# Performance work log

Hardware: AMD Instinct MI355X
Metric: run time of the kernel (lower is better)

## Reference

```python
import jax, jax.numpy as jnp
import numpy as np

B, L, D, H = 8, 2048, 1024, 1024
BASE_LR, BASE_WD = 0.01, 0.9


def setup_inputs() -> dict:
    key = jax.random.key(0)
    ks = jax.random.split(key, 8)
    s = 1.0 / np.sqrt(D)
    return {
        "x": jax.random.normal(ks[0], (B, L, D), jnp.float32),
        "hidden": jax.random.normal(ks[1], (B, D, H), jnp.float32),
        "log_base_lr": jnp.array([np.log(BASE_LR)], jnp.float32),
        "w_lr": jax.random.normal(ks[2], (D, 1), jnp.float32) * s,
        "b_lr": jnp.zeros((1,), jnp.float32),
        "log_base_wd": jnp.array([np.log(BASE_WD)], jnp.float32),
        "w_wd": jax.random.normal(ks[3], (D, 1), jnp.float32) * s,
        "b_wd": jnp.zeros((1,), jnp.float32),
        "w_q": jax.random.normal(ks[4], (D, H), jnp.float32) * s,
        "b_q": jnp.zeros((H,), jnp.float32),
        "w_k": jax.random.normal(ks[5], (D, H), jnp.float32) * s,
        "b_k": jnp.zeros((H,), jnp.float32),
        "w_v": jax.random.normal(ks[6], (D, D), jnp.float32) * s,
        "b_v": jnp.zeros((D,), jnp.float32),
    }


def reference(x, hidden, log_base_lr, w_lr, b_lr, log_base_wd, w_wd, b_wd,
              w_q, b_q, w_k, b_k, w_v, b_v):
    batch, length, dim = x.shape
    W_prev = hidden  # [b, d, h]
    query = x @ w_q + b_q                     # [b, l, h]
    key = x @ w_k + b_k                       # [b, l, h]
    value = x @ w_v + b_v                     # [b, l, d]
    lr = jnp.exp(log_base_lr) * jax.nn.sigmoid((x @ w_lr + b_lr)[..., 0])  # [b, l]
    # log(1 - base_wd * sigmoid(.)) via log1p for stability; same math.
    log_wd = jnp.log1p(-jnp.exp(log_base_wd) * jax.nn.sigmoid((x @ w_wd + b_wd)[..., 0]))  # [b, l]
    wd_cross = jnp.exp(jnp.cumsum(log_wd, axis=1))  # [b, l]
    # inner-chunk decay: entry [b, m, l] = exp(sum_{j=m+1..l} log_wd[b, j]) for l >= m
    tri = jnp.triu(jnp.broadcast_to(log_wd[:, None, :], (batch, length, length)), k=1)
    wd_inner = jnp.triu(jnp.exp(jnp.cumsum(tri, axis=2)))  # [b, l, l]
    kq = jnp.einsum('bld,bmd->blm', key, query)            # [b, l, m]
    mask_kq = kq * wd_inner
    WpK_V = jnp.einsum('bdh,blh->bld', W_prev, key) - value  # [b, l, d]
    y_inner = -jnp.einsum('bld,bl,blm->bmd', WpK_V, lr, mask_kq)
    y_cross = jnp.einsum('bdh,blh,bl->bld', W_prev, query, wd_cross)
    y = y_inner + y_cross
    W_next_inner = -jnp.einsum('bld,bl,blh->bdh', WpK_V, lr * wd_inner[:, :, -1], key)
    W_next_cross = W_prev * wd_cross[:, -1][:, None, None]
    W_next = W_next_inner + W_next_cross
    return y, W_next
```

## Files before the change

kernel.cpp:

```cpp
#include <hip/hip_runtime.h>
#include <stdint.h>

#define BB 8
#define LL 2048
#define DD 1024
#define HH 1024
#define BL (BB*LL)

typedef __attribute__((ext_vector_type(8))) short short8;
typedef __attribute__((ext_vector_type(4))) float f32x4;

__device__ __forceinline__ unsigned short f2bf(float f) {
  unsigned int x = __float_as_uint(f);
  unsigned int r = (x + 0x7fffu + ((x >> 16) & 1u)) >> 16;
  return (unsigned short)r;
}
__device__ __forceinline__ float bf2f(unsigned short u) {
  return __uint_as_float(((unsigned int)u) << 16);
}

__device__ __forceinline__ void stage16(const unsigned short* g, unsigned short* l) {
  __builtin_amdgcn_global_load_lds((const __attribute__((address_space(1))) void*)g,
                                   (__attribute__((address_space(3))) void*)l,
                                   16, 0, 0);
}

template<int N> struct WaitVm;
#define WVM(N) template<> struct WaitVm<N> { \
  static __device__ __forceinline__ void w() { \
    asm volatile("s_waitcnt vmcnt(" #N ")" ::: "memory"); } };
WVM(0) WVM(6) WVM(8) WVM(12)
#undef WVM

template<int MI, int PD>
struct __align__(16) Smem3 {
  unsigned short a[PD+1][MI*2048];
  unsigned short b[PD+1][16384];
};

template<int MI>
__device__ __forceinline__ void acc_init2(f32x4 (&acc)[MI][4]) {
#pragma unroll
  for (int i = 0; i < MI; ++i)
#pragma unroll
    for (int j = 0; j < 4; ++j)
      acc[i][j] = (f32x4){0.f, 0.f, 0.f, 0.f};
}

template<int MI, int PD, class FA, class FB>
__device__ __forceinline__ void gemm3_core(FA srcA, FB srcB, int NK,
                                           Smem3<MI,PD>* sm, f32x4 (&acc)[MI][4]) {
  constexpr int NB  = PD + 1;
  constexpr int APW = MI / 2;
  constexpr int LPW = APW + 4;
  const int lane = threadIdx.x & 63;
  const int wave = threadIdx.x >> 6;
  const int srow = lane >> 3;
  const int scol = ((lane & 7) ^ srow) * 8;
  const int fk = (lane >> 4) * 8;
  const int fr = lane & 15;
  const int fx = fr & 7;
  const int mwr = (wave >> 2) * (MI * 16);
  const int nwr = (wave & 3) * 64;

  auto STAGE = [&](int p, int kt) {
#pragma unroll
    for (int r = 0; r < APW; ++r) {
      const int chunk = wave * APW + r;
      stage16(srcA(chunk * 8 + srow, kt) + scol, &sm->a[p][chunk * 512]);
    }
#pragma unroll
    for (int r = 0; r < 4; ++r) {
      const int chunk = wave * 4 + r;
      stage16(srcB(chunk * 8 + srow, kt) + scol, &sm->b[p][chunk * 512]);
    }
  };
  auto COMPUTE = [&](int p) {
    const unsigned short* pa  = sm->a[p];
    const unsigned short* pbp = sm->b[p];
#pragma unroll
    for (int kk = 0; kk < 64; kk += 32) {
      const int kc = ((((kk + fk) >> 3) ^ fx) << 3);
      short8 af[MI], bfv[4];
#pragma unroll
      for (int i = 0; i < MI; ++i)
        af[i] = *(const short8*)&pa[(mwr + i*16 + fr) * 64 + kc];
#pragma unroll
      for (int j = 0; j < 4; ++j)
        bfv[j] = *(const short8*)&pbp[(nwr + j*16 + fr) * 64 + kc];
#pragma unroll
      for (int i = 0; i < MI; ++i)
#pragma unroll
        for (int j = 0; j < 4; ++j)
          acc[i][j] = __builtin_amdgcn_mfma_f32_16x16x32_bf16(af[i], bfv[j], acc[i][j], 0, 0, 0);
    }
  };

#pragma unroll
  for (int d = 0; d < PD; ++d) STAGE(d, d);
  int pc = 0;
  int ps = PD % NB;
  for (int kt = 0; kt < NK; ++kt) {
    if (kt + PD < NK) {
      STAGE(ps, kt + PD);
      ps = (ps + 1 == NB) ? 0 : ps + 1;
      WaitVm<PD * LPW>::w();
    } else if (PD == 2 && kt + PD == NK) {
      WaitVm<LPW>::w();
    } else {
      WaitVm<0>::w();
    }
    __builtin_amdgcn_s_barrier();
    __builtin_amdgcn_sched_barrier(0);
    COMPUTE(pc);
    pc = (pc + 1 == NB) ? 0 : pc + 1;
    __builtin_amdgcn_s_barrier();
  }
}

template<int MI, typename F>
__device__ __forceinline__ void epi2(const f32x4 (&acc)[MI][4], F body) {
  const int lane = threadIdx.x & 63;
  const int wave = threadIdx.x >> 6;
  const int mwr = (wave >> 2) * (MI * 16), nwr = (wave & 3) * 64;
#pragma unroll
  for (int i = 0; i < MI; ++i)
#pragma unroll
    for (int j = 0; j < 4; ++j)
#pragma unroll
      for (int jj = 0; jj < 4; ++jj) {
        const int rr = mwr + i * 16 + ((lane >> 4) << 2) + jj;
        const int cc = nwr + j * 16 + (lane & 15);
        body(rr, cc, acc[i][j][jj]);
      }
}


__global__ void k_prep_x(const float* __restrict__ x, const float* __restrict__ wlr,
                         const float* __restrict__ wwd, unsigned short* __restrict__ xb,
                         float* __restrict__ lrlog, float* __restrict__ wdlog) {
  const int wave = threadIdx.x >> 6, lane = threadIdx.x & 63;
  const int row = blockIdx.x * 4 + wave;
  const float* xr = x + (size_t)row * DD;
  float s1 = 0.f, s2 = 0.f;
#pragma unroll
  for (int ch = 0; ch < 4; ++ch) {
    const int col = ch * 256 + lane * 4;
    float4 v = *(const float4*)(xr + col);
    float4 a = *(const float4*)(wlr + col);
    float4 b = *(const float4*)(wwd + col);
    s1 += v.x*a.x + v.y*a.y + v.z*a.z + v.w*a.w;
    s2 += v.x*b.x + v.y*b.y + v.z*b.z + v.w*b.w;
    uint2 u;
    u.x = (unsigned)f2bf(v.x) | ((unsigned)f2bf(v.y) << 16);
    u.y = (unsigned)f2bf(v.z) | ((unsigned)f2bf(v.w) << 16);
    *(uint2*)(xb + (size_t)row * DD + col) = u;
  }
#pragma unroll
  for (int off = 32; off > 0; off >>= 1) {
    s1 += __shfl_down(s1, off);
    s2 += __shfl_down(s2, off);
  }
  if (lane == 0) { lrlog[row] = s1; wdlog[row] = s2; }
}

__global__ void k_prep_w(const float* __restrict__ wq, const float* __restrict__ wk,
                         const float* __restrict__ wv, unsigned short* __restrict__ wqt,
                         unsigned short* __restrict__ wkt, unsigned short* __restrict__ wvtn,
                         unsigned short* __restrict__ wkr) {
  const int idx = blockIdx.x * 256 + threadIdx.x;
  if (blockIdx.z == 3) { wkr[idx] = f2bf(wk[idx]); return; }
  const int k = idx >> 10, n = idx & 1023;
  const float* src = (blockIdx.z == 0) ? wq : (blockIdx.z == 1) ? wk : wv;
  unsigned short* dst = (blockIdx.z == 0) ? wqt : (blockIdx.z == 1) ? wkt : wvtn;
  float v = src[(size_t)k * 1024 + n];
  if (blockIdx.z == 2) v = -v;
  dst[(size_t)n * 1024 + k] = f2bf(v);
}

__global__ void k_prep_h(const float* __restrict__ hid, unsigned short* __restrict__ wpb) {
  const size_t i = ((size_t)blockIdx.x * 256 + threadIdx.x) * 4;
  float4 v = *(const float4*)(hid + i);
  uint2 u;
  u.x = (unsigned)f2bf(v.x) | ((unsigned)f2bf(v.y) << 16);
  u.y = (unsigned)f2bf(v.z) | ((unsigned)f2bf(v.w) << 16);
  *(uint2*)(wpb + i) = u;
}

__global__ void k_bias2(const unsigned short* __restrict__ wpb, const float* __restrict__ bk,
                        const float* __restrict__ bv, float* __restrict__ bias2) {
  const int wave = threadIdx.x >> 6, lane = threadIdx.x & 63;
  const int row = blockIdx.x * 4 + wave;
  const unsigned short* wr = wpb + (size_t)row * HH;
  float s = 0.f;
#pragma unroll
  for (int ch = 0; ch < 4; ++ch) {
    const int col = ch * 256 + lane * 4;
    float4 a = *(const float4*)(bk + col);
    ushort4 u = *(const ushort4*)(wr + col);
    s += a.x * bf2f(u.x) + a.y * bf2f(u.y) + a.z * bf2f(u.z) + a.w * bf2f(u.w);
  }
#pragma unroll
  for (int off = 32; off > 0; off >>= 1) s += __shfl_down(s, off);
  if (lane == 0) bias2[row] = s - bv[row & 1023];
}

__global__ void k_scan(const float* __restrict__ lrlog, const float* __restrict__ wdlog,
                       const float* __restrict__ lbl, const float* __restrict__ blr,
                       const float* __restrict__ lbw, const float* __restrict__ bwd,
                       float* __restrict__ lr, float* __restrict__ c,
                       float* __restrict__ s, float* __restrict__ ecl) {
  const int b = blockIdx.x, t = threadIdx.x;
  __shared__ float sums[256];
  const float elr = expf(lbl[0]);
  const float ewd = expf(lbw[0]);
  const float blr0 = blr[0], bwd0 = bwd[0];
  float lw[8];
  const float* wb = wdlog + (size_t)b * LL + t * 8;
  float tot = 0.f;
#pragma unroll
  for (int i = 0; i < 8; ++i) {
    float z = wb[i] + bwd0;
    float sig = 1.f / (1.f + expf(-z));
    tot += log1pf(-ewd * sig);
    lw[i] = tot;
  }
  sums[t] = tot;
  __syncthreads();
  for (int off = 1; off < 256; off <<= 1) {
    float v = (t >= off) ? sums[t - off] : 0.f;
    __syncthreads();
    sums[t] += v;
    __syncthreads();
  }
  const float prev = (t > 0) ? sums[t - 1] : 0.f;
  const float ctot = sums[255];
  const float* lb = lrlog + (size_t)b * LL + t * 8;
#pragma unroll
  for (int i = 0; i < 8; ++i) {
    const int idx = b * LL + t * 8 + i;
    const float ci = prev + lw[i];
    c[idx] = ci;
    float zl = lb[i] + blr0;
    float lri = elr / (1.f + expf(-zl));
    lr[idx] = lri;
    s[idx] = lri * expf(ctot - ci);
  }
  if (t == 0) ecl[b] = expf(ctot);
}


__global__ __launch_bounds__(512, 2) void k3_gemm_m2(const unsigned short* __restrict__ wpb,
    const unsigned short* __restrict__ wkr, const unsigned short* __restrict__ wvtn,
    unsigned short* __restrict__ w2t) {
  __shared__ Smem3<4,2> sm;
  const int b = blockIdx.x;
  const int mt = blockIdx.y & 7, nt = blockIdx.y >> 3;
  const int m0 = mt * 128, n0 = nt * 256;
  f32x4 acc[4][4]; acc_init2<4>(acc);
  gemm3_core<4,2>(
    [&](int r, int kt) { return wpb + (size_t)b * DD * HH + (size_t)(m0 + r) * HH + kt * 64; },
    [&](int r, int kt) { return wkr + (size_t)(n0 + r) * HH + kt * 64; },
    HH / 64, &sm, acc);
  epi2<4>(acc, [&](int rr, int cc, float av) {
    const size_t gi = (size_t)(m0 + rr) * DD + (n0 + cc);
    w2t[(size_t)b * DD * DD + gi] = f2bf(av + bf2f(wvtn[gi]));
  });
}

__global__ __launch_bounds__(512, 2) void k3_gemm_q(const unsigned short* __restrict__ xb,
    const unsigned short* __restrict__ wt, const float* __restrict__ bias,
    const float* __restrict__ c, unsigned short* __restrict__ outb,
    unsigned short* __restrict__ q2b) {
  __shared__ Smem3<8,1> sm;
  const int mt = blockIdx.x * 8 + (blockIdx.y & 7);
  const int nt = blockIdx.y >> 3;
  const int m0 = mt * 256, n0 = nt * 256;
  f32x4 acc[8][4]; acc_init2<8>(acc);
  gemm3_core<8,1>(
    [&](int r, int kt) { return xb + (size_t)(m0 + r) * DD + kt * 64; },
    [&](int r, int kt) { return wt + (size_t)(n0 + r) * DD + kt * 64; },
    DD / 64, &sm, acc);
  epi2<8>(acc, [&](int rr, int cc, float av) {
    const int row = m0 + rr, col = n0 + cc;
    const float v = av + bias[col];
    outb[(size_t)row * HH + col] = f2bf(v);
    q2b[(size_t)row * HH + col] = f2bf(v * __expf(c[row]));
  });
}

__global__ __launch_bounds__(512, 2) void k3_gemm_k(const unsigned short* __restrict__ xb,
    const unsigned short* __restrict__ wt, const float* __restrict__ bias,
    const float* __restrict__ s, unsigned short* __restrict__ kb,
    unsigned short* __restrict__ k2t) {
  __shared__ Smem3<8,1> sm;
  const int mt = blockIdx.x * 8 + (blockIdx.y & 7);
  const int nt = blockIdx.y >> 3;
  const int m0 = mt * 256, n0 = nt * 256;
  f32x4 acc[8][4]; acc_init2<8>(acc);
  gemm3_core<8,1>(
    [&](int r, int kt) { return xb + (size_t)(m0 + r) * DD + kt * 64; },
    [&](int r, int kt) { return wt + (size_t)(n0 + r) * DD + kt * 64; },
    DD / 64, &sm, acc);
  const int lane = threadIdx.x & 63, wave = threadIdx.x >> 6;
  const int mwr = (wave >> 2) * 128, nwr = (wave & 3) * 64;
#pragma unroll
  for (int i = 0; i < 8; ++i)
#pragma unroll
    for (int j = 0; j < 4; ++j) {
      const int col = n0 + nwr + j*16 + (lane & 15);
      const float bias_c = bias[col];
      const int row0 = m0 + mwr + i*16 + ((lane >> 4) << 2);
      const int b = row0 >> 11, ml0 = row0 & 2047;
      unsigned short tmp[4];
#pragma unroll
      for (int jj = 0; jj < 4; ++jj) {
        float v = acc[i][j][jj] + bias_c;
        kb[(size_t)(row0 + jj) * HH + col] = f2bf(v);
        tmp[jj] = f2bf(v * s[row0 + jj]);
      }
      uint2 u;
      u.x = (unsigned)tmp[0] | ((unsigned)tmp[1] << 16);
      u.y = (unsigned)tmp[2] | ((unsigned)tmp[3] << 16);
      *(uint2*)&k2t[((size_t)b * HH + col) * LL + ml0] = u;
    }
}

__global__ __launch_bounds__(512, 2) void k3_gemm_u(const unsigned short* __restrict__ xb,
    const unsigned short* __restrict__ w2t, const float* __restrict__ bias2,
    unsigned short* __restrict__ ut) {
  __shared__ Smem3<8,1> sm;
  const int b = blockIdx.x;
  const int mt = blockIdx.x * 8 + (blockIdx.y & 7);
  const int nt = blockIdx.y >> 3;
  const int m0 = mt * 256, n0 = nt * 256;
  f32x4 acc[8][4]; acc_init2<8>(acc);
  gemm3_core<8,1>(
    [&](int r, int kt) { return xb + (size_t)(m0 + r) * DD + kt * 64; },
    [&](int r, int kt) { return w2t + (size_t)b * DD * DD + (size_t)(n0 + r) * DD + kt * 64; },
    DD / 64, &sm, acc);
  const int lane = threadIdx.x & 63, wave = threadIdx.x >> 6;
  const int mwr = (wave >> 2) * 128, nwr = (wave & 3) * 64;
#pragma unroll
  for (int i = 0; i < 8; ++i)
#pragma unroll
    for (int j = 0; j < 4; ++j) {
      const int col = n0 + nwr + j*16 + (lane & 15);
      const float b2c = bias2[b * DD + col];
      const int row0 = m0 + mwr + i*16 + ((lane >> 4) << 2);
      const int ml0 = row0 & 2047;
      unsigned short tmp[4];
#pragma unroll
      for (int jj = 0; jj < 4; ++jj) tmp[jj] = f2bf(acc[i][j][jj] + b2c);
      uint2 u;
      u.x = (unsigned)tmp[0] | ((unsigned)tmp[1] << 16);
      u.y = (unsigned)tmp[2] | ((unsigned)tmp[3] << 16);
      *(uint2*)&ut[((size_t)b * DD + col) * LL + ml0] = u;
    }
}

__global__ __launch_bounds__(512, 2) void k3_gemm_p(const unsigned short* __restrict__ qb,
    const unsigned short* __restrict__ kb, const float* __restrict__ lr,
    const float* __restrict__ c, unsigned short* __restrict__ pb) {
  __shared__ Smem3<4,2> sm;
  const int b = blockIdx.x;
  const int t = blockIdx.y;
  int r = (int)((sqrtf(4.f * (float)t + 1.f) - 1.f) * 0.5f);
  while ((r + 1) * (r + 2) <= t) ++r;
  while (r * (r + 1) > t) --r;
  const int u = t - r * (r + 1);
  const int mt = 2 * r + (u > r ? 1 : 0);
  const int nt2 = (u > r) ? (u - r - 1) : u;
  const int base = b * LL;
  const int m0 = mt * 128, n0 = nt2 * 256;
  f32x4 acc[4][4]; acc_init2<4>(acc);
  gemm3_core<4,2>(
    [&](int rr, int kt) { return qb + (size_t)(base + m0 + rr) * HH + kt * 64; },
    [&](int rr, int kt) { return kb + (size_t)(base + n0 + rr) * HH + kt * 64; },
    HH / 64, &sm, acc);
  epi2<4>(acc, [&](int rr, int cc, float av) {
    const int m = m0 + rr, l = n0 + cc;
    float v = 0.f;
    if (l <= m) v = -av * lr[base + l] * __expf(c[base + m] - c[base + l]);
    pb[((size_t)base + m) * LL + l] = f2bf(v);
  });
}

__global__ __launch_bounds__(512, 2) void k3_gemm_y(const unsigned short* __restrict__ pb,
    const unsigned short* __restrict__ ut, const unsigned short* __restrict__ q2b,
    const unsigned short* __restrict__ wpb, float* __restrict__ out) {
  __shared__ Smem3<4,2> sm;
  const int b = blockIdx.x;
  const int mt = 15 - (blockIdx.y & 15);
  const int nt = blockIdx.y >> 4;
  const int m0 = mt * 128, n0 = nt * 256;
  const int NK1 = (mt + 1) * 2;
  f32x4 acc[4][4]; acc_init2<4>(acc);
  gemm3_core<4,2>(
    [&](int r, int kt) {
      return (kt < NK1) ? pb + (size_t)b * LL * LL + (size_t)(m0 + r) * LL + kt * 64
                        : q2b + ((size_t)b * LL + m0 + r) * HH + (kt - NK1) * 64;
    },
    [&](int r, int kt) {
      return (kt < NK1) ? ut + (size_t)b * DD * LL + (size_t)(n0 + r) * LL + kt * 64
                        : wpb + (size_t)b * DD * HH + (size_t)(n0 + r) * HH + (kt - NK1) * 64;
    },
    NK1 + 16, &sm, acc);
  epi2<4>(acc, [&](int rr, int cc, float av) {
    out[((size_t)b * LL + m0 + rr) * DD + (n0 + cc)] = av;
  });
}

__global__ __launch_bounds__(512, 2) void k3_gemm_wn(const unsigned short* __restrict__ ut,
    const unsigned short* __restrict__ k2t, const float* __restrict__ hid,
    const float* __restrict__ ecl, float* __restrict__ out2) {
  __shared__ Smem3<4,2> sm;
  const int b = blockIdx.x;
  const int mt = blockIdx.y & 7, nt = blockIdx.y >> 3;
  const int m0 = mt * 128, n0 = nt * 256;
  f32x4 acc[4][4]; acc_init2<4>(acc);
  gemm3_core<4,2>(
    [&](int r, int kt) { return ut + (size_t)b * DD * LL + (size_t)(m0 + r) * LL + kt * 64; },
    [&](int r, int kt) { return k2t + (size_t)b * HH * LL + (size_t)(n0 + r) * LL + kt * 64; },
    LL / 64, &sm, acc);
  const float eclb = ecl[b];
  epi2<4>(acc, [&](int rr, int cc, float av) {
    const size_t gi = ((size_t)b * DD + (m0 + rr)) * HH + (n0 + cc);
    out2[gi] = -av + eclb * hid[gi];
  });
}


extern "C" void kernel_launch(void* const* d_in, const int* in_sizes, int n_in,
                              void* d_out, int out_size, void* d_ws, size_t ws_size,
                              hipStream_t stream) {
  (void)in_sizes; (void)n_in; (void)out_size; (void)ws_size;
  const float* x   = (const float*)d_in[0];
  const float* hid = (const float*)d_in[1];
  const float* lbl = (const float*)d_in[2];
  const float* wlr = (const float*)d_in[3];
  const float* blr = (const float*)d_in[4];
  const float* lbw = (const float*)d_in[5];
  const float* wwd = (const float*)d_in[6];
  const float* bwd = (const float*)d_in[7];
  const float* wq  = (const float*)d_in[8];
  const float* bq  = (const float*)d_in[9];
  const float* wk  = (const float*)d_in[10];
  const float* bk  = (const float*)d_in[11];
  const float* wv  = (const float*)d_in[12];
  const float* bv  = (const float*)d_in[13];
  float* out = (float*)d_out;

  char* w = (char*)d_ws;
  constexpr size_t SZ_XB  = (size_t)BL * DD * 2;
  constexpr size_t SZ_QB  = (size_t)BL * HH * 2;
  constexpr size_t SZ_KB  = (size_t)BL * HH * 2;
  constexpr size_t SZ_K2T = (size_t)BB * HH * LL * 2;
  constexpr size_t SZ_UT  = (size_t)BB * DD * LL * 2;
  constexpr size_t SZ_PB  = (size_t)BB * LL * LL * 2;
  constexpr size_t SZ_WT  = (size_t)DD * HH * 2;
  constexpr size_t SZ_WPB = (size_t)BB * DD * HH * 2;
  constexpr size_t SZ_V16 = (size_t)BL * 4;

  size_t off = 0;
  unsigned short* xb   = (unsigned short*)(w + off); off += SZ_XB;
  unsigned short* qb   = (unsigned short*)(w + off); off += SZ_QB;
  unsigned short* kb   = (unsigned short*)(w + off); off += SZ_KB;
  unsigned short* k2t  = (unsigned short*)(w + off); off += SZ_K2T;
  unsigned short* ut   = (unsigned short*)(w + off); off += SZ_UT;
  unsigned short* pb   = (unsigned short*)(w + off); off += SZ_PB;
  unsigned short* wqt  = (unsigned short*)(w + off); off += SZ_WT;
  unsigned short* wkt  = (unsigned short*)(w + off); off += SZ_WT;
  unsigned short* wvtn = (unsigned short*)(w + off); off += SZ_WT;
  unsigned short* wpb  = (unsigned short*)(w + off); off += SZ_WPB;
  float* lrlog = (float*)(w + off); off += SZ_V16;
  float* wdlog = (float*)(w + off); off += SZ_V16;
  float* lr    = (float*)(w + off); off += SZ_V16;
  float* c     = (float*)(w + off); off += SZ_V16;
  float* s     = (float*)(w + off); off += SZ_V16;
  float* ecl   = (float*)(w + off); off += 256;
  float* bias2 = (float*)(w + off); off += (size_t)BB * DD * 4;

  unsigned short* w2t = pb;
  unsigned short* wkr = pb + (size_t)BB * DD * DD;

  unsigned short* q2b = (unsigned short*)(out + (size_t)BL * DD);
  float* out2 = out + (size_t)BL * DD;

  k_prep_x<<<dim3(BL / 4), 256, 0, stream>>>(x, wlr, wwd, xb, lrlog, wdlog);
  k_prep_w<<<dim3(4096, 1, 4), 256, 0, stream>>>(wq, wk, wv, wqt, wkt, wvtn, wkr);
  k_prep_h<<<dim3((unsigned)((size_t)BB * DD * HH / 1024)), 256, 0, stream>>>(hid, wpb);
  k_scan<<<dim3(BB), 256, 0, stream>>>(lrlog, wdlog, lbl, blr, lbw, bwd, lr, c, s, ecl);
  k_bias2<<<dim3(BB * DD / 4), 256, 0, stream>>>(wpb, bk, bv, bias2);

  k3_gemm_m2<<<dim3(8, 32), 512, 0, stream>>>(wpb, wkr, wvtn, w2t);
  k3_gemm_q<<<dim3(8, 32), 512, 0, stream>>>(xb, wqt, bq, c, qb, q2b);
  k3_gemm_k<<<dim3(8, 32), 512, 0, stream>>>(xb, wkt, bk, s, kb, k2t);
  k3_gemm_u<<<dim3(8, 32), 512, 0, stream>>>(xb, w2t, bias2, ut);
  k3_gemm_p<<<dim3(8, 72), 512, 0, stream>>>(qb, kb, lr, c, pb);
  k3_gemm_y<<<dim3(8, 64), 512, 0, stream>>>(pb, ut, q2b, wpb, out);
  k3_gemm_wn<<<dim3(8, 32), 512, 0, stream>>>(ut, k2t, hid, ecl, out2);
}
```

Measured before the change: 615.9 us.

## Replace GEMM core with 256x256 tiled 8-wave ping-pong pipeline across all GEMMs

```diff
diff --git a/kernel.cpp b/kernel.cpp
--- a/kernel.cpp
+++ b/kernel.cpp
@@ -25,34 +25,23 @@
                                    16, 0, 0);
 }
 
-template<int N> struct WaitVm;
-#define WVM(N) template<> struct WaitVm<N> { \
-  static __device__ __forceinline__ void w() { \
-    asm volatile("s_waitcnt vmcnt(" #N ")" ::: "memory"); } };
-WVM(0) WVM(6) WVM(8) WVM(12)
-#undef WVM
-
-template<int MI, int PD>
-struct __align__(16) Smem3 {
-  unsigned short a[PD+1][MI*2048];
-  unsigned short b[PD+1][16384];
+struct __align__(16) Smem8 {
+  unsigned short a[2][16384];
+  unsigned short b[2][16384];
 };
-
-template<int MI>
-__device__ __forceinline__ void acc_init2(f32x4 (&acc)[MI][4]) {
-#pragma unroll
-  for (int i = 0; i < MI; ++i)
+static_assert(sizeof(Smem8) == 131072, "LDS size");
+
+__device__ __forceinline__ void acc_init8(f32x4 (&acc)[8][4]) {
+#pragma unroll
+  for (int i = 0; i < 8; ++i)
 #pragma unroll
     for (int j = 0; j < 4; ++j)
       acc[i][j] = (f32x4){0.f, 0.f, 0.f, 0.f};
 }
 
-template<int MI, int PD, class FA, class FB>
-__device__ __forceinline__ void gemm3_core(FA srcA, FB srcB, int NK,
-                                           Smem3<MI,PD>* sm, f32x4 (&acc)[MI][4]) {
-  constexpr int NB  = PD + 1;
-  constexpr int APW = MI / 2;
-  constexpr int LPW = APW + 4;
+template<class FA, class FB>
+__device__ __forceinline__ void gemm8_core(FA srcA, FB srcB, int NK,
+                                           Smem8* sm, f32x4 (&acc)[8][4]) {
   const int lane = threadIdx.x & 63;
   const int wave = threadIdx.x >> 6;
   const int srow = lane >> 3;
@@ -60,79 +49,104 @@
   const int fk = (lane >> 4) * 8;
   const int fr = lane & 15;
   const int fx = fr & 7;
-  const int mwr = (wave >> 2) * (MI * 16);
+  const int mwr = (wave >> 2) * 128;
   const int nwr = (wave & 3) * 64;
-
-  auto STAGE = [&](int p, int kt) {
-#pragma unroll
-    for (int r = 0; r < APW; ++r) {
-      const int chunk = wave * APW + r;
-      stage16(srcA(chunk * 8 + srow, kt) + scol, &sm->a[p][chunk * 512]);
-    }
-#pragma unroll
-    for (int r = 0; r < 4; ++r) {
-      const int chunk = wave * 4 + r;
-      stage16(srcB(chunk * 8 + srow, kt) + scol, &sm->b[p][chunk * 512]);
-    }
+  const int cA0 = (wave < 4) ? 2 * wave : 2 * wave + 8;
+  const int cA1 = cA0 + 8;
+  const int cB0 = (wave >> 1) * 8 + 2 * (wave & 1);
+  const int cB1 = cB0 + 4;
+
+  auto SA = [&](int p, int kt, int c) {
+    stage16(srcA(c * 8 + srow, kt) + scol, &sm->a[p][c * 512]);
+    stage16(srcA(c * 8 + 8 + srow, kt) + scol, &sm->a[p][(c + 1) * 512]);
   };
-  auto COMPUTE = [&](int p) {
-    const unsigned short* pa  = sm->a[p];
-    const unsigned short* pbp = sm->b[p];
-#pragma unroll
-    for (int kk = 0; kk < 64; kk += 32) {
-      const int kc = ((((kk + fk) >> 3) ^ fx) << 3);
-      short8 af[MI], bfv[4];
-#pragma unroll
-      for (int i = 0; i < MI; ++i)
-        af[i] = *(const short8*)&pa[(mwr + i*16 + fr) * 64 + kc];
-#pragma unroll
-      for (int j = 0; j < 4; ++j)
-        bfv[j] = *(const short8*)&pbp[(nwr + j*16 + fr) * 64 + kc];
-#pragma unroll
-      for (int i = 0; i < MI; ++i)
-#pragma unroll
-        for (int j = 0; j < 4; ++j)
-          acc[i][j] = __builtin_amdgcn_mfma_f32_16x16x32_bf16(af[i], bfv[j], acc[i][j], 0, 0, 0);
-    }
+  auto SB = [&](int p, int kt, int c) {
+    stage16(srcB(c * 8 + srow, kt) + scol, &sm->b[p][c * 512]);
+    stage16(srcB(c * 8 + 8 + srow, kt) + scol, &sm->b[p][(c + 1) * 512]);
   };
-
-#pragma unroll
-  for (int d = 0; d < PD; ++d) STAGE(d, d);
-  int pc = 0;
-  int ps = PD % NB;
-  for (int kt = 0; kt < NK; ++kt) {
-    if (kt + PD < NK) {
-      STAGE(ps, kt + PD);
-      ps = (ps + 1 == NB) ? 0 : ps + 1;
-      WaitVm<PD * LPW>::w();
-    } else if (PD == 2 && kt + PD == NK) {
-      WaitVm<LPW>::w();
-    } else {
-      WaitVm<0>::w();
-    }
-    __builtin_amdgcn_s_barrier();
-    __builtin_amdgcn_sched_barrier(0);
-    COMPUTE(pc);
-    pc = (pc + 1 == NB) ? 0 : pc + 1;
-    __builtin_amdgcn_s_barrier();
-  }
-}
-
-template<int MI, typename F>
-__device__ __forceinline__ void epi2(const f32x4 (&acc)[MI][4], F body) {
+  short8 af[4][2], bfv[2][2];
+  auto LDA = [&](int p, int ih) {
+#pragma unroll
+    for (int i = 0; i < 4; ++i)
+#pragma unroll
+      for (int kk = 0; kk < 2; ++kk) {
+        const int kc = ((((kk * 32 + fk) >> 3) ^ fx) << 3);
+        af[i][kk] = *(const short8*)&sm->a[p][(mwr + ih * 64 + i * 16 + fr) * 64 + kc];
+      }
+  };
+  auto LDB = [&](int p, int jh) {
+#pragma unroll
+    for (int j = 0; j < 2; ++j)
+#pragma unroll
+      for (int kk = 0; kk < 2; ++kk) {
+        const int kc = ((((kk * 32 + fk) >> 3) ^ fx) << 3);
+        bfv[j][kk] = *(const short8*)&sm->b[p][(nwr + jh * 32 + j * 16 + fr) * 64 + kc];
+      }
+  };
+  auto MM = [&](int ih, int jh) {
+#pragma unroll
+    for (int i = 0; i < 4; ++i)
+#pragma unroll
+      for (int j = 0; j < 2; ++j)
+#pragma unroll
+        for (int kk = 0; kk < 2; ++kk)
+          acc[ih * 4 + i][jh * 2 + j] = __builtin_amdgcn_mfma_f32_16x16x32_bf16(
+              af[i][kk], bfv[j][kk], acc[ih * 4 + i][jh * 2 + j], 0, 0, 0);
+  };
+
+#define PH(IH, JH, ...) do { \
+    __VA_ARGS__ \
+    __builtin_amdgcn_sched_barrier(0); \
+    __builtin_amdgcn_s_barrier(); \
+    asm volatile("s_waitcnt lgkmcnt(0)" ::: "memory"); \
+    __builtin_amdgcn_sched_barrier(0); \
+    __builtin_amdgcn_s_setprio(1); \
+    MM(IH, JH); \
+    __builtin_amdgcn_s_setprio(0); \
+    __builtin_amdgcn_sched_barrier(0); \
+    __builtin_amdgcn_s_barrier(); \
+    __builtin_amdgcn_sched_barrier(0); \
+  } while (0)
+
+  if (NK > 1) {
+    SA(0, 0, cA0); SA(0, 0, cA1); SB(0, 0, cB0); SB(0, 0, cB1);
+    SB(1, 1, cB0); SA(1, 1, cA0);
+    asm volatile("s_waitcnt vmcnt(4)" ::: "memory");
+  } else {
+    SA(0, 0, cA0); SA(0, 0, cA1); SB(0, 0, cB0); SB(0, 0, cB1);
+    asm volatile("s_waitcnt vmcnt(0)" ::: "memory");
+  }
+  __builtin_amdgcn_sched_barrier(0);
+  __builtin_amdgcn_s_barrier();
+  __builtin_amdgcn_sched_barrier(0);
+
+  for (int t = 0; t < NK; ++t) {
+    const int p = t & 1, po = p ^ 1;
+    const bool s1 = (t + 1 < NK), s2 = (t + 2 < NK);
+    PH(0, 0, LDA(p, 0); LDB(p, 0); if (s1) SA(po, t + 1, cA1); );
+    PH(1, 0, LDA(p, 1);            if (s1) SB(po, t + 1, cB1); );
+    PH(0, 1, LDA(p, 0); LDB(p, 1); if (s2) SB(p, t + 2, cB0); );
+    PH(1, 1, LDA(p, 1);
+             if (s2) SA(p, t + 2, cA0);
+             if (s2)      { asm volatile("s_waitcnt vmcnt(4)" ::: "memory"); }
+             else if (s1) { asm volatile("s_waitcnt vmcnt(0)" ::: "memory"); } );
+  }
+#undef PH
+}
+
+template<typename F>
+__device__ __forceinline__ void epi8(const f32x4 (&acc)[8][4], F body) {
   const int lane = threadIdx.x & 63;
   const int wave = threadIdx.x >> 6;
-  const int mwr = (wave >> 2) * (MI * 16), nwr = (wave & 3) * 64;
-#pragma unroll
-  for (int i = 0; i < MI; ++i)
+  const int mwr = (wave >> 2) * 128, nwr = (wave & 3) * 64;
+#pragma unroll
+  for (int i = 0; i < 8; ++i)
 #pragma unroll
     for (int j = 0; j < 4; ++j)
 #pragma unroll
-      for (int jj = 0; jj < 4; ++jj) {
-        const int rr = mwr + i * 16 + ((lane >> 4) << 2) + jj;
-        const int cc = nwr + j * 16 + (lane & 15);
-        body(rr, cc, acc[i][j][jj]);
-      }
+      for (int jj = 0; jj < 4; ++jj)
+        body(mwr + i * 16 + ((lane >> 4) << 2) + jj,
+             nwr + j * 16 + (lane & 15), acc[i][j][jj]);
 }
 
 
@@ -250,67 +264,81 @@
 }
 
 
-__global__ __launch_bounds__(512, 2) void k3_gemm_m2(const unsigned short* __restrict__ wpb,
+__global__ __launch_bounds__(512, 2) void k8_gemm_m2(const unsigned short* __restrict__ wpb,
     const unsigned short* __restrict__ wkr, const unsigned short* __restrict__ wvtn,
     unsigned short* __restrict__ w2t) {
-  __shared__ Smem3<4,2> sm;
+  __shared__ Smem8 sm;
   const int b = blockIdx.x;
-  const int mt = blockIdx.y & 7, nt = blockIdx.y >> 3;
-  const int m0 = mt * 128, n0 = nt * 256;
-  f32x4 acc[4][4]; acc_init2<4>(acc);
-  gemm3_core<4,2>(
+  const int mt = blockIdx.y & 3, nt = blockIdx.y >> 2;
+  const int m0 = mt * 256, n0 = nt * 256;
+  f32x4 acc[8][4]; acc_init8(acc);
+  gemm8_core(
     [&](int r, int kt) { return wpb + (size_t)b * DD * HH + (size_t)(m0 + r) * HH + kt * 64; },
     [&](int r, int kt) { return wkr + (size_t)(n0 + r) * HH + kt * 64; },
     HH / 64, &sm, acc);
-  epi2<4>(acc, [&](int rr, int cc, float av) {
+  epi8(acc, [&](int rr, int cc, float av) {
     const size_t gi = (size_t)(m0 + rr) * DD + (n0 + cc);
     w2t[(size_t)b * DD * DD + gi] = f2bf(av + bf2f(wvtn[gi]));
   });
 }
 
-__global__ __launch_bounds__(512, 2) void k3_gemm_q(const unsigned short* __restrict__ xb,
+__global__ __launch_bounds__(512, 2) void k8_gemm_q(const unsigned short* __restrict__ xb,
     const unsigned short* __restrict__ wt, const float* __restrict__ bias,
     const float* __restrict__ c, unsigned short* __restrict__ outb,
     unsigned short* __restrict__ q2b) {
-  __shared__ Smem3<8,1> sm;
+  __shared__ Smem8 sm;
   const int mt = blockIdx.x * 8 + (blockIdx.y & 7);
   const int nt = blockIdx.y >> 3;
   const int m0 = mt * 256, n0 = nt * 256;
-  f32x4 acc[8][4]; acc_init2<8>(acc);
-  gemm3_core<8,1>(
-    [&](int r, int kt) { return xb + (size_t)(m0 + r) * DD + kt * 64; },
-    [&](int r, int kt) { return wt + (size_t)(n0 + r) * DD + kt * 64; },
-    DD / 64, &sm, acc);
-  epi2<8>(acc, [&](int rr, int cc, float av) {
-    const int row = m0 + rr, col = n0 + cc;
-    const float v = av + bias[col];
-    outb[(size_t)row * HH + col] = f2bf(v);
-    q2b[(size_t)row * HH + col] = f2bf(v * __expf(c[row]));
-  });
-}
-
-__global__ __launch_bounds__(512, 2) void k3_gemm_k(const unsigned short* __restrict__ xb,
-    const unsigned short* __restrict__ wt, const float* __restrict__ bias,
-    const float* __restrict__ s, unsigned short* __restrict__ kb,
-    unsigned short* __restrict__ k2t) {
-  __shared__ Smem3<8,1> sm;
-  const int mt = blockIdx.x * 8 + (blockIdx.y & 7);
-  const int nt = blockIdx.y >> 3;
-  const int m0 = mt * 256, n0 = nt * 256;
-  f32x4 acc[8][4]; acc_init2<8>(acc);
-  gemm3_core<8,1>(
+  f32x4 acc[8][4]; acc_init8(acc);
+  gemm8_core(
     [&](int r, int kt) { return xb + (size_t)(m0 + r) * DD + kt * 64; },
     [&](int r, int kt) { return wt + (size_t)(n0 + r) * DD + kt * 64; },
     DD / 64, &sm, acc);
   const int lane = threadIdx.x & 63, wave = threadIdx.x >> 6;
   const int mwr = (wave >> 2) * 128, nwr = (wave & 3) * 64;
+  float er[8][4];
 #pragma unroll
   for (int i = 0; i < 8; ++i)
 #pragma unroll
+    for (int jj = 0; jj < 4; ++jj)
+      er[i][jj] = __expf(c[m0 + mwr + i * 16 + ((lane >> 4) << 2) + jj]);
+#pragma unroll
+  for (int i = 0; i < 8; ++i)
+#pragma unroll
+    for (int j = 0; j < 4; ++j)
+#pragma unroll
+      for (int jj = 0; jj < 4; ++jj) {
+        const int row = m0 + mwr + i * 16 + ((lane >> 4) << 2) + jj;
+        const int col = n0 + nwr + j * 16 + (lane & 15);
+        const float v = acc[i][j][jj] + bias[col];
+        outb[(size_t)row * HH + col] = f2bf(v);
+        q2b[(size_t)row * HH + col] = f2bf(v * er[i][jj]);
+      }
+}
+
+__global__ __launch_bounds__(512, 2) void k8_gemm_k(const unsigned short* __restrict__ xb,
+    const unsigned short* __restrict__ wt, const float* __restrict__ bias,
+    const float* __restrict__ s, unsigned short* __restrict__ kb,
+    unsigned short* __restrict__ k2t) {
+  __shared__ Smem8 sm;
+  const int mt = blockIdx.x * 8 + (blockIdx.y & 7);
+  const int nt = blockIdx.y >> 3;
+  const int m0 = mt * 256, n0 = nt * 256;
+  f32x4 acc[8][4]; acc_init8(acc);
+  gemm8_core(
+    [&](int r, int kt) { return xb + (size_t)(m0 + r) * DD + kt * 64; },
+    [&](int r, int kt) { return wt + (size_t)(n0 + r) * DD + kt * 64; },
+    DD / 64, &sm, acc);
+  const int lane = threadIdx.x & 63, wave = threadIdx.x >> 6;
+  const int mwr = (wave >> 2) * 128, nwr = (wave & 3) * 64;
+#pragma unroll
+  for (int i = 0; i < 8; ++i)
+#pragma unroll
     for (int j = 0; j < 4; ++j) {
-      const int col = n0 + nwr + j*16 + (lane & 15);
+      const int col = n0 + nwr + j * 16 + (lane & 15);
       const float bias_c = bias[col];
-      const int row0 = m0 + mwr + i*16 + ((lane >> 4) << 2);
+      const int row0 = m0 + mwr + i * 16 + ((lane >> 4) << 2);
       const int b = row0 >> 11, ml0 = row0 & 2047;
       unsigned short tmp[4];
 #pragma unroll
@@ -326,16 +354,16 @@
     }
 }
 
-__global__ __launch_bounds__(512, 2) void k3_gemm_u(const unsigned short* __restrict__ xb,
+__global__ __launch_bounds__(512, 2) void k8_gemm_u(const unsigned short* __restrict__ xb,
     const unsigned short* __restrict__ w2t, const float* __restrict__ bias2,
     unsigned short* __restrict__ ut) {
-  __shared__ Smem3<8,1> sm;
+  __shared__ Smem8 sm;
   const int b = blockIdx.x;
   const int mt = blockIdx.x * 8 + (blockIdx.y & 7);
   const int nt = blockIdx.y >> 3;
   const int m0 = mt * 256, n0 = nt * 256;
-  f32x4 acc[8][4]; acc_init2<8>(acc);
-  gemm3_core<8,1>(
+  f32x4 acc[8][4]; acc_init8(acc);
+  gemm8_core(
     [&](int r, int kt) { return xb + (size_t)(m0 + r) * DD + kt * 64; },
     [&](int r, int kt) { return w2t + (size_t)b * DD * DD + (size_t)(n0 + r) * DD + kt * 64; },
     DD / 64, &sm, acc);
@@ -345,9 +373,9 @@
   for (int i = 0; i < 8; ++i)
 #pragma unroll
     for (int j = 0; j < 4; ++j) {
-      const int col = n0 + nwr + j*16 + (lane & 15);
+      const int col = n0 + nwr + j * 16 + (lane & 15);
       const float b2c = bias2[b * DD + col];
-      const int row0 = m0 + mwr + i*16 + ((lane >> 4) << 2);
+      const int row0 = m0 + mwr + i * 16 + ((lane >> 4) << 2);
       const int ml0 = row0 & 2047;
       unsigned short tmp[4];
 #pragma unroll
@@ -359,44 +387,71 @@
     }
 }
 
-__global__ __launch_bounds__(512, 2) void k3_gemm_p(const unsigned short* __restrict__ qb,
+__global__ __launch_bounds__(512, 2) void k8_gemm_p(const unsigned short* __restrict__ qb,
     const unsigned short* __restrict__ kb, const float* __restrict__ lr,
     const float* __restrict__ c, unsigned short* __restrict__ pb) {
-  __shared__ Smem3<4,2> sm;
+  __shared__ Smem8 sm;
   const int b = blockIdx.x;
   const int t = blockIdx.y;
-  int r = (int)((sqrtf(4.f * (float)t + 1.f) - 1.f) * 0.5f);
-  while ((r + 1) * (r + 2) <= t) ++r;
-  while (r * (r + 1) > t) --r;
-  const int u = t - r * (r + 1);
-  const int mt = 2 * r + (u > r ? 1 : 0);
-  const int nt2 = (u > r) ? (u - r - 1) : u;
+  int mt = (int)((sqrtf(8.f * (float)t + 1.f) - 1.f) * 0.5f);
+  while ((mt + 1) * (mt + 2) / 2 <= t) ++mt;
+  while (mt * (mt + 1) / 2 > t) --mt;
+  const int nt = t - mt * (mt + 1) / 2;
   const int base = b * LL;
-  const int m0 = mt * 128, n0 = nt2 * 256;
-  f32x4 acc[4][4]; acc_init2<4>(acc);
-  gemm3_core<4,2>(
+  const int m0 = mt * 256, n0 = nt * 256;
+  f32x4 acc[8][4]; acc_init8(acc);
+  gemm8_core(
     [&](int rr, int kt) { return qb + (size_t)(base + m0 + rr) * HH + kt * 64; },
     [&](int rr, int kt) { return kb + (size_t)(base + n0 + rr) * HH + kt * 64; },
     HH / 64, &sm, acc);
-  epi2<4>(acc, [&](int rr, int cc, float av) {
-    const int m = m0 + rr, l = n0 + cc;
-    float v = 0.f;
-    if (l <= m) v = -av * lr[base + l] * __expf(c[base + m] - c[base + l]);
-    pb[((size_t)base + m) * LL + l] = f2bf(v);
-  });
-}
-
-__global__ __launch_bounds__(512, 2) void k3_gemm_y(const unsigned short* __restrict__ pb,
+  const int lane = threadIdx.x & 63, wave = threadIdx.x >> 6;
+  const int mwr = (wave >> 2) * 128, nwr = (wave & 3) * 64;
+  if (nt != mt) {
+    const float cref = c[base + m0];
+    float er[8][4], fc[4];
+#pragma unroll
+    for (int i = 0; i < 8; ++i)
+#pragma unroll
+      for (int jj = 0; jj < 4; ++jj)
+        er[i][jj] = __expf(c[base + m0 + mwr + i * 16 + ((lane >> 4) << 2) + jj] - cref);
+#pragma unroll
+    for (int j = 0; j < 4; ++j) {
+      const int l = n0 + nwr + j * 16 + (lane & 15);
+      fc[j] = lr[base + l] * __expf(cref - c[base + l]);
+    }
+#pragma unroll
+    for (int i = 0; i < 8; ++i)
+#pragma unroll
+      for (int j = 0; j < 4; ++j) {
+        const int l = n0 + nwr + j * 16 + (lane & 15);
+        const int row0 = m0 + mwr + i * 16 + ((lane >> 4) << 2);
+#pragma unroll
+        for (int jj = 0; jj < 4; ++jj) {
+          const float v = -acc[i][j][jj] * er[i][jj] * fc[j];
+          pb[((size_t)base + row0 + jj) * LL + l] = f2bf(v);
+        }
+      }
+  } else {
+    epi8(acc, [&](int rr, int cc, float av) {
+      const int m = m0 + rr, l = n0 + cc;
+      float v = 0.f;
+      if (l <= m) v = -av * lr[base + l] * __expf(c[base + m] - c[base + l]);
+      pb[((size_t)base + m) * LL + l] = f2bf(v);
+    });
+  }
+}
+
+__global__ __launch_bounds__(512, 2) void k8_gemm_y(const unsigned short* __restrict__ pb,
     const unsigned short* __restrict__ ut, const unsigned short* __restrict__ q2b,
     const unsigned short* __restrict__ wpb, float* __restrict__ out) {
-  __shared__ Smem3<4,2> sm;
+  __shared__ Smem8 sm;
   const int b = blockIdx.x;
-  const int mt = 15 - (blockIdx.y & 15);
-  const int nt = blockIdx.y >> 4;
-  const int m0 = mt * 128, n0 = nt * 256;
-  const int NK1 = (mt + 1) * 2;
-  f32x4 acc[4][4]; acc_init2<4>(acc);
-  gemm3_core<4,2>(
+  const int mt = blockIdx.y & 7;
+  const int nt = blockIdx.y >> 3;
+  const int m0 = mt * 256, n0 = nt * 256;
+  const int NK1 = (mt + 1) * 4;
+  f32x4 acc[8][4]; acc_init8(acc);
+  gemm8_core(
     [&](int r, int kt) {
       return (kt < NK1) ? pb + (size_t)b * LL * LL + (size_t)(m0 + r) * LL + kt * 64
                         : q2b + ((size_t)b * LL + m0 + r) * HH + (kt - NK1) * 64;
@@ -406,25 +461,25 @@
                         : wpb + (size_t)b * DD * HH + (size_t)(n0 + r) * HH + (kt - NK1) * 64;
     },
     NK1 + 16, &sm, acc);
-  epi2<4>(acc, [&](int rr, int cc, float av) {
+  epi8(acc, [&](int rr, int cc, float av) {
     out[((size_t)b * LL + m0 + rr) * DD + (n0 + cc)] = av;
   });
 }
 
-__global__ __launch_bounds__(512, 2) void k3_gemm_wn(const unsigned short* __restrict__ ut,
+__global__ __launch_bounds__(512, 2) void k8_gemm_wn(const unsigned short* __restrict__ ut,
     const unsigned short* __restrict__ k2t, const float* __restrict__ hid,
     const float* __restrict__ ecl, float* __restrict__ out2) {
-  __shared__ Smem3<4,2> sm;
+  __shared__ Smem8 sm;
   const int b = blockIdx.x;
-  const int mt = blockIdx.y & 7, nt = blockIdx.y >> 3;
-  const int m0 = mt * 128, n0 = nt * 256;
-  f32x4 acc[4][4]; acc_init2<4>(acc);
-  gemm3_core<4,2>(
+  const int mt = blockIdx.y & 3, nt = blockIdx.y >> 2;
+  const int m0 = mt * 256, n0 = nt * 256;
+  f32x4 acc[8][4]; acc_init8(acc);
+  gemm8_core(
     [&](int r, int kt) { return ut + (size_t)b * DD * LL + (size_t)(m0 + r) * LL + kt * 64; },
     [&](int r, int kt) { return k2t + (size_t)b * HH * LL + (size_t)(n0 + r) * LL + kt * 64; },
     LL / 64, &sm, acc);
   const float eclb = ecl[b];
-  epi2<4>(acc, [&](int rr, int cc, float av) {
+  epi8(acc, [&](int rr, int cc, float av) {
     const size_t gi = ((size_t)b * DD + (m0 + rr)) * HH + (n0 + cc);
     out2[gi] = -av + eclb * hid[gi];
   });
@@ -493,11 +548,11 @@
   k_scan<<<dim3(BB), 256, 0, stream>>>(lrlog, wdlog, lbl, blr, lbw, bwd, lr, c, s, ecl);
   k_bias2<<<dim3(BB * DD / 4), 256, 0, stream>>>(wpb, bk, bv, bias2);
 
-  k3_gemm_m2<<<dim3(8, 32), 512, 0, stream>>>(wpb, wkr, wvtn, w2t);
-  k3_gemm_q<<<dim3(8, 32), 512, 0, stream>>>(xb, wqt, bq, c, qb, q2b);
-  k3_gemm_k<<<dim3(8, 32), 512, 0, stream>>>(xb, wkt, bk, s, kb, k2t);
-  k3_gemm_u<<<dim3(8, 32), 512, 0, stream>>>(xb, w2t, bias2, ut);
-  k3_gemm_p<<<dim3(8, 72), 512, 0, stream>>>(qb, kb, lr, c, pb);
-  k3_gemm_y<<<dim3(8, 64), 512, 0, stream>>>(pb, ut, q2b, wpb, out);
-  k3_gemm_wn<<<dim3(8, 32), 512, 0, stream>>>(ut, k2t, hid, ecl, out2);
-}
+  k8_gemm_m2<<<dim3(8, 16), 512, 0, stream>>>(wpb, wkr, wvtn, w2t);
+  k8_gemm_q<<<dim3(8, 32), 512, 0, stream>>>(xb, wqt, bq, c, qb, q2b);
+  k8_gemm_k<<<dim3(8, 32), 512, 0, stream>>>(xb, wkt, bk, s, kb, k2t);
+  k8_gemm_u<<<dim3(8, 32), 512, 0, stream>>>(xb, w2t, bias2, ut);
+  k8_gemm_p<<<dim3(8, 36), 512, 0, stream>>>(qb, kb, lr, c, pb);
+  k8_gemm_y<<<dim3(8, 32), 512, 0, stream>>>(pb, ut, q2b, wpb, out);
+  k8_gemm_wn<<<dim3(8, 16), 512, 0, stream>>>(ut, k2t, hid, ecl, out2);
+}
```

Result: slower. 649.4 us (+5.4%).
